# Performance work log

Measured on AMD Instinct MI355X. Metric: run time of the kernel, lower is better.

The kernel has to match this reference:

```python
import jax, jax.numpy as jnp
import numpy as np

# TripletSTDP hyperparameters (match torch defaults / init_kwargs)
TAU_PLUS = 20.0
TAU_MINUS = 20.0
TAU_X = 101.0
TAU_Y = 114.0
A_PLUS = 0.005
A_MINUS = 0.00525
A_TRIP_PLUS = 0.0001
A_TRIP_MINUS = 0.0001
DT = 1.0

B, T, N_PRE, N_POST = 32, 512, 1024, 1024


def setup_inputs() -> dict:
    key = jax.random.key(0)
    k1, k2, k3 = jax.random.split(key, 3)
    pre_spikes = jax.random.uniform(k1, (B, T, N_PRE), dtype=jnp.float32)
    post_spikes = jax.random.uniform(k2, (B, T, N_POST), dtype=jnp.float32)
    weights = jax.random.uniform(k3, (N_PRE, N_POST), dtype=jnp.float32)
    return {"pre_spikes": pre_spikes, "post_spikes": post_spikes, "weights": weights}


def reference(pre_spikes, post_spikes, weights):
    batch, time_steps, n_pre = pre_spikes.shape
    n_post = post_spikes.shape[-1]
    d_plus = jnp.exp(jnp.asarray(-DT / TAU_PLUS, dtype=pre_spikes.dtype))
    d_x = jnp.exp(jnp.asarray(-DT / TAU_X, dtype=pre_spikes.dtype))
    d_minus = jnp.exp(jnp.asarray(-DT / TAU_MINUS, dtype=pre_spikes.dtype))
    d_y = jnp.exp(jnp.asarray(-DT / TAU_Y, dtype=pre_spikes.dtype))
    inv_b = 1.0 / batch

    def step(carry, xs):
        r1, r2, o1, o2, wu = carry
        pre_t, post_t = xs  # [B, n_pre], [B, n_post]
        r1 = r1 * d_plus
        r2 = r2 * d_x
        o1 = o1 * d_minus
        o2 = o2 * d_y
        # LTP: (a_plus*r1 + a_tp*r1*r2) outer post_t, mean over batch
        wu = wu + jnp.einsum('bp,bq->pq', A_PLUS * r1 + A_TRIP_PLUS * (r1 * r2), post_t) * inv_b
        # LTD: pre_t outer (a_minus*o1 + a_tm*o1*o2), mean over batch, negated
        wu = wu - jnp.einsum('bp,bq->pq', pre_t, A_MINUS * o1 + A_TRIP_MINUS * (o1 * o2)) * inv_b
        return (r1 + pre_t, r2 + pre_t, o1 + post_t, o2 + post_t, wu), None

    init = (
        jnp.zeros((batch, n_pre), dtype=pre_spikes.dtype),
        jnp.zeros((batch, n_pre), dtype=pre_spikes.dtype),
        jnp.zeros((batch, n_post), dtype=post_spikes.dtype),
        jnp.zeros((batch, n_post), dtype=post_spikes.dtype),
        jnp.zeros_like(weights),
    )
    xs = (jnp.swapaxes(pre_spikes, 0, 1), jnp.swapaxes(post_spikes, 0, 1))  # [T,B,*]
    (r1, r2, o1, o2, wu), _ = jax.lax.scan(step, init, xs)
    return wu / time_steps
```

## Files before the change

kernel.cpp:

```cpp
#include <hip/hip_runtime.h>
#include <cstdint>
#include <cmath>

#define BDIM 256

constexpr int Bsz = 32;
constexpr int Tt  = 512;
constexpr int Nn  = 1024;
constexpr int SEG = 16;
constexpr int SLEN = 32;
constexpr int SPLITS = 8;
constexpr int NKT = (2 * Bsz * Tt / 32) / SPLITS;
constexpr float A_PLUS  = 0.005f;
constexpr float A_MINUS = 0.00525f;
constexpr float A_TP    = 0.0001f;
constexpr float A_TM    = 0.0001f;

typedef __attribute__((ext_vector_type(8))) short short8;
typedef __attribute__((ext_vector_type(4))) float float4v;

__device__ __forceinline__ unsigned short f2bf(float f) {
  unsigned u = __float_as_uint(f);
  u += 0x7fffu + ((u >> 16) & 1u);
  return (unsigned short)(u >> 16);
}

__global__ __launch_bounds__(BDIM) void trace_kernel(
    const float* __restrict__ pre, const float* __restrict__ post,
    unsigned short* __restrict__ Abuf, unsigned short* __restrict__ Bbuf,
    float d_plus, float d_x, float d_minus, float d_y)
{
  int nb   = blockIdx.x & 63;
  int b    = (blockIdx.x >> 6) & 31;
  int side = blockIdx.x >> 11;
  int tid  = threadIdx.x;
  int seg  = tid >> 4;
  int nl   = tid & 15;
  int n    = nb * 16 + nl;

  const float* sp = (side ? post : pre) + (size_t)b * Tt * Nn + n;
  float da = side ? d_minus : d_plus;
  float db = side ? d_y     : d_x;
  float c1 = side ? -A_MINUS : A_PLUS;
  float c2 = side ? -A_TM    : A_TP;
  unsigned short* dbuf = side ? Bbuf : Abuf;
  int sw = (nl >> 1) & 3;
  int t0 = seg * SLEN;

  __shared__ __align__(16) unsigned short op[SEG][2][16][32];
  float* lds1 = (float*)&op[0][0][0][0];
  float* lds2 = lds1 + SEG * 16;

  float s[SLEN];
#pragma unroll
  for (int j = 0; j < SLEN; ++j) s[j] = sp[(size_t)(t0 + j) * Nn];

  float l1 = 0.f, l2 = 0.f;
#pragma unroll
  for (int j = 0; j < SLEN; ++j) {
    l1 = l1 * da + s[j];
    l2 = l2 * db + s[j];
  }

  float dL1 = da, dL2 = db;
#pragma unroll
  for (int q = 0; q < 5; ++q) { dL1 *= dL1; dL2 *= dL2; }

  lds1[seg * 16 + nl] = l1; lds2[seg * 16 + nl] = l2;
  __syncthreads();
  float tr1 = 0.f, tr2 = 0.f;
#pragma unroll
  for (int m = 0; m < SEG - 1; ++m) {
    if (m < seg) {
      tr1 = tr1 * dL1 + lds1[m * 16 + nl];
      tr2 = tr2 * dL2 + lds2[m * 16 + nl];
    }
  }
  __syncthreads();

#pragma unroll
  for (int g2 = 0; g2 < SLEN / 16; ++g2) {
    short8 w0[2], w1[2];
#pragma unroll
    for (int j = 0; j < 16; ++j) {
      float sv = s[g2 * 16 + j];
      tr1 *= da; tr2 *= db;
      float tv = c1 * tr1 + c2 * (tr1 * tr2);
      unsigned short bs = f2bf(sv);
      unsigned short bt = f2bf(tv);
      unsigned short h0 = side ? bs : bt;
      unsigned short h1 = side ? bt : bs;
      w0[j >> 3][j & 7] = (short)h0;
      w1[j >> 3][j & 7] = (short)h1;
      tr1 += sv; tr2 += sv;
    }
    int slotbase = 2 * g2;
#pragma unroll
    for (int i = 0; i < 2; ++i) {
      int slot = slotbase + i;
      *(short8*)&op[seg][0][nl][(slot ^ sw) * 8] = w0[i];
      *(short8*)&op[seg][1][nl][(slot ^ sw) * 8] = w1[i];
    }
  }
  __syncthreads();

  int wid = tid >> 6, lane = tid & 63;
  const unsigned short* opb = &op[0][0][0][0];
  size_t bb = (size_t)b * 16;
#pragma unroll
  for (int st = 0; st < 8; ++st) {
    int r  = wid * 8 + st;
    int sg = r >> 1;
    int dX = r & 1;
    size_t ge = ((size_t)(dX * 512) + bb + sg) * 32768
              + (size_t)(nb >> 3) * 4096 + (size_t)(nb & 7) * 512 + lane * 8;
    *(short8*)(dbuf + ge) = *(const short8*)(opb + (size_t)r * 512 + lane * 8);
  }
}

#define GLL(gp, lp)                                                         \
  __builtin_amdgcn_global_load_lds(                                         \
      (const __attribute__((address_space(1))) unsigned int*)(gp),          \
      (__attribute__((address_space(3))) unsigned int*)(lp), 16, 0, 0)

#define WAITCNT_VM8 0xF78
#define WAITCNT_VM4 0xF74
#define WAITCNT_VM0 0xF70

__global__ __launch_bounds__(BDIM) void gemm_kernel(
    const unsigned short* __restrict__ Abuf, const unsigned short* __restrict__ Bbuf,
    float* __restrict__ partials)
{
  __shared__ unsigned short smem[3 * 8192];
  int tid  = threadIdx.x;
  int s    = blockIdx.x & 7;
  int tile = blockIdx.x >> 3;
  int pt   = tile & 7;
  int qt   = tile >> 3;

  float4v acc[4][4];
#pragma unroll
  for (int i = 0; i < 4; ++i)
#pragma unroll
    for (int j = 0; j < 4; ++j) acc[i][j] = (float4v){0.f, 0.f, 0.f, 0.f};

  int wid = tid >> 6, lane = tid & 63;
  int wr = wid >> 1, wc = wid & 1;
  int rA = wr * 64 + (lane & 15);
  int rB = wc * 64 + (lane & 15);
  int kg = (((lane >> 4) ^ ((lane >> 1) & 3)) * 8);

  const unsigned short* ga = Abuf + ((size_t)(s * NKT) * 8 + pt) * 4096 + tid * 8;
  const unsigned short* gb = Bbuf + ((size_t)(s * NKT) * 8 + qt) * 4096 + tid * 8;

#define ISSUE(kt_) do {                                                     \
    unsigned short* sb_ = smem + ((kt_) % 3) * 8192;                        \
    const unsigned short* a_ = ga + (size_t)(kt_) * 8 * 4096;               \
    const unsigned short* b_ = gb + (size_t)(kt_) * 8 * 4096;               \
    GLL(a_,        sb_ + tid * 8);                                          \
    GLL(a_ + 2048, sb_ + 2048 + tid * 8);                                   \
    GLL(b_,        sb_ + 4096 + tid * 8);                                   \
    GLL(b_ + 2048, sb_ + 6144 + tid * 8);                                   \
  } while (0)

  ISSUE(0);
  ISSUE(1);

  for (int kt = 0; kt < NKT; ++kt) {
    if (kt + 2 < NKT) {
      ISSUE(kt + 2);
      __builtin_amdgcn_s_waitcnt(WAITCNT_VM8);
    } else if (kt + 2 == NKT) {
      __builtin_amdgcn_s_waitcnt(WAITCNT_VM4);
    } else {
      __builtin_amdgcn_s_waitcnt(WAITCNT_VM0);
    }
    __builtin_amdgcn_s_barrier();

    const unsigned short* sb = smem + (kt % 3) * 8192;
    short8 af[4], bfv[4];
#pragma unroll
    for (int mi = 0; mi < 4; ++mi)
      af[mi] = *(const short8*)(sb + (rA + mi * 16) * 32 + kg);
#pragma unroll
    for (int ni = 0; ni < 4; ++ni)
      bfv[ni] = *(const short8*)(sb + 4096 + (rB + ni * 16) * 32 + kg);
#pragma unroll
    for (int mi = 0; mi < 4; ++mi)
#pragma unroll
      for (int ni = 0; ni < 4; ++ni)
        acc[mi][ni] = __builtin_amdgcn_mfma_f32_16x16x32_bf16(af[mi], bfv[ni], acc[mi][ni], 0, 0, 0);
  }

  float* po = partials + (size_t)s * Nn * Nn;
#pragma unroll
  for (int mi = 0; mi < 4; ++mi)
#pragma unroll
    for (int r = 0; r < 4; ++r) {
      int row = pt * 128 + wr * 64 + mi * 16 + (lane >> 4) * 4 + r;
#pragma unroll
      for (int ni = 0; ni < 4; ++ni) {
        int col = qt * 128 + wc * 64 + ni * 16 + (lane & 15);
        po[(size_t)row * Nn + col] = acc[mi][ni][r];
      }
    }
#undef ISSUE
}

__global__ __launch_bounds__(BDIM) void reduce_kernel(
    const float4v* __restrict__ partials, float4v* __restrict__ out, int S, float scale)
{
  size_t i = (size_t)blockIdx.x * BDIM + threadIdx.x;
  float4v v = (float4v){0.f, 0.f, 0.f, 0.f};
  for (int s = 0; s < S; ++s) v += partials[(size_t)s * (Nn * Nn / 4) + i];
  out[i] = v * scale;
}

extern "C" void kernel_launch(void* const* d_in, const int* in_sizes, int n_in,
                              void* d_out, int out_size, void* d_ws, size_t ws_size,
                              hipStream_t stream)
{
  const float* pre  = (const float*)d_in[0];
  const float* post = (const float*)d_in[1];
  float4v* out = (float4v*)d_out;
  char* ws = (char*)d_ws;

  size_t sizeAB = (size_t)2 * Bsz * Tt * Nn * 2;

  float* partials = (float*)ws;
  unsigned short* Abuf = (unsigned short*)(ws + (size_t)SPLITS * Nn * Nn * 4);
  unsigned short* Bbuf = (unsigned short*)(ws + (size_t)SPLITS * Nn * Nn * 4 + sizeAB);

  float d_plus  = expf(-1.0f / 20.0f);
  float d_x     = expf(-1.0f / 101.0f);
  float d_minus = expf(-1.0f / 20.0f);
  float d_y     = expf(-1.0f / 114.0f);

  trace_kernel<<<2 * Bsz * Nn / 16, BDIM, 0, stream>>>(
      pre, post, Abuf, Bbuf, d_plus, d_x, d_minus, d_y);
  gemm_kernel<<<64 * SPLITS, BDIM, 0, stream>>>(Abuf, Bbuf, partials);
  reduce_kernel<<<(Nn * Nn / 4) / BDIM, BDIM, 0, stream>>>(
      (const float4v*)partials, out, SPLITS, 1.0f / (float)(Bsz * Tt));
}
```

Baseline: 256.2 us.

## Widen trace blocks to 32 neurons with longer time segments, two-pass LDS staging

The trace kernel now gives each block 32 neurons and 8 time segments of 64 steps, instead of 16 neurons and 16 segments of 32. Global reads become wider (128 B per row per segment) and the serial cross-segment prefix shrinks. Each thread produces its 64 steps in two halves that reuse the same LDS staging buffer, with barriers between the halves, before writing the bf16 operand tiles in the layout the GEMM expects. The price is 64 floats of register state per thread, hence launch_bounds(256,4), plus an extra barrier round and half as many blocks.

```diff
diff --git a/kernel.cpp b/kernel.cpp
--- a/kernel.cpp
+++ b/kernel.cpp
@@ -7,8 +7,8 @@
 constexpr int Bsz = 32;
 constexpr int Tt  = 512;
 constexpr int Nn  = 1024;
-constexpr int SEG = 16;
-constexpr int SLEN = 32;
+constexpr int SEG = 8;
+constexpr int SLEN = 64;
 constexpr int SPLITS = 8;
 constexpr int NKT = (2 * Bsz * Tt / 32) / SPLITS;
 constexpr float A_PLUS  = 0.005f;
@@ -25,18 +25,18 @@
   return (unsigned short)(u >> 16);
 }
 
-__global__ __launch_bounds__(BDIM) void trace_kernel(
+__global__ __launch_bounds__(BDIM, 4) void trace_kernel(
     const float* __restrict__ pre, const float* __restrict__ post,
     unsigned short* __restrict__ Abuf, unsigned short* __restrict__ Bbuf,
     float d_plus, float d_x, float d_minus, float d_y)
 {
-  int nb   = blockIdx.x & 63;
-  int b    = (blockIdx.x >> 6) & 31;
-  int side = blockIdx.x >> 11;
+  int nb   = blockIdx.x & 31;
+  int b    = (blockIdx.x >> 5) & 31;
+  int side = blockIdx.x >> 10;
   int tid  = threadIdx.x;
-  int seg  = tid >> 4;
-  int nl   = tid & 15;
-  int n    = nb * 16 + nl;
+  int seg  = tid >> 5;
+  int nl   = tid & 31;
+  int n    = nb * 32 + nl;
 
   const float* sp = (side ? post : pre) + (size_t)b * Tt * Nn + n;
   float da = side ? d_minus : d_plus;
@@ -47,9 +47,9 @@
   int sw = (nl >> 1) & 3;
   int t0 = seg * SLEN;
 
-  __shared__ __align__(16) unsigned short op[SEG][2][16][32];
+  __shared__ __align__(16) unsigned short op[SEG][2][32][32];
   float* lds1 = (float*)&op[0][0][0][0];
-  float* lds2 = lds1 + SEG * 16;
+  float* lds2 = lds1 + SEG * 32;
 
   float s[SLEN];
 #pragma unroll
@@ -64,57 +64,64 @@
 
   float dL1 = da, dL2 = db;
 #pragma unroll
-  for (int q = 0; q < 5; ++q) { dL1 *= dL1; dL2 *= dL2; }
-
-  lds1[seg * 16 + nl] = l1; lds2[seg * 16 + nl] = l2;
+  for (int q = 0; q < 6; ++q) { dL1 *= dL1; dL2 *= dL2; }
+
+  lds1[seg * 32 + nl] = l1; lds2[seg * 32 + nl] = l2;
   __syncthreads();
   float tr1 = 0.f, tr2 = 0.f;
 #pragma unroll
   for (int m = 0; m < SEG - 1; ++m) {
     if (m < seg) {
-      tr1 = tr1 * dL1 + lds1[m * 16 + nl];
-      tr2 = tr2 * dL2 + lds2[m * 16 + nl];
+      tr1 = tr1 * dL1 + lds1[m * 32 + nl];
+      tr2 = tr2 * dL2 + lds2[m * 32 + nl];
     }
   }
   __syncthreads();
 
-#pragma unroll
-  for (int g2 = 0; g2 < SLEN / 16; ++g2) {
-    short8 w0[2], w1[2];
-#pragma unroll
-    for (int j = 0; j < 16; ++j) {
-      float sv = s[g2 * 16 + j];
-      tr1 *= da; tr2 *= db;
-      float tv = c1 * tr1 + c2 * (tr1 * tr2);
-      unsigned short bs = f2bf(sv);
-      unsigned short bt = f2bf(tv);
-      unsigned short h0 = side ? bs : bt;
-      unsigned short h1 = side ? bt : bs;
-      w0[j >> 3][j & 7] = (short)h0;
-      w1[j >> 3][j & 7] = (short)h1;
-      tr1 += sv; tr2 += sv;
-    }
-    int slotbase = 2 * g2;
-#pragma unroll
-    for (int i = 0; i < 2; ++i) {
-      int slot = slotbase + i;
-      *(short8*)&op[seg][0][nl][(slot ^ sw) * 8] = w0[i];
-      *(short8*)&op[seg][1][nl][(slot ^ sw) * 8] = w1[i];
-    }
-  }
-  __syncthreads();
-
   int wid = tid >> 6, lane = tid & 63;
-  const unsigned short* opb = &op[0][0][0][0];
-  size_t bb = (size_t)b * 16;
-#pragma unroll
-  for (int st = 0; st < 8; ++st) {
-    int r  = wid * 8 + st;
-    int sg = r >> 1;
-    int dX = r & 1;
-    size_t ge = ((size_t)(dX * 512) + bb + sg) * 32768
-              + (size_t)(nb >> 3) * 4096 + (size_t)(nb & 7) * 512 + lane * 8;
-    *(short8*)(dbuf + ge) = *(const short8*)(opb + (size_t)r * 512 + lane * 8);
+
+#pragma unroll
+  for (int r = 0; r < 2; ++r) {
+#pragma unroll
+    for (int g2 = 0; g2 < 2; ++g2) {
+      short8 w0[2], w1[2];
+#pragma unroll
+      for (int j = 0; j < 16; ++j) {
+        float sv = s[r * 32 + g2 * 16 + j];
+        tr1 *= da; tr2 *= db;
+        float tv = c1 * tr1 + c2 * (tr1 * tr2);
+        unsigned short bs = f2bf(sv);
+        unsigned short bt = f2bf(tv);
+        unsigned short h0 = side ? bs : bt;
+        unsigned short h1 = side ? bt : bs;
+        w0[j >> 3][j & 7] = (short)h0;
+        w1[j >> 3][j & 7] = (short)h1;
+        tr1 += sv; tr2 += sv;
+      }
+#pragma unroll
+      for (int i = 0; i < 2; ++i) {
+        int slot = g2 * 2 + i;
+        *(short8*)&op[seg][0][nl][(slot ^ sw) * 8] = w0[i];
+        *(short8*)&op[seg][1][nl][(slot ^ sw) * 8] = w1[i];
+      }
+    }
+    __syncthreads();
+
+    const unsigned short* opb = &op[0][0][0][0];
+#pragma unroll
+    for (int i = 0; i < 4; ++i) {
+      int rid = wid * 4 + i;
+      int sg  = rid >> 1;
+      int dX  = rid & 1;
+      size_t kt = (size_t)(dX * 512 + b * 16 + sg * 2 + r);
+      size_t ge = (kt * 8 + (size_t)(nb >> 2)) * 4096 + (size_t)(nb & 3) * 1024;
+#pragma unroll
+      for (int h = 0; h < 2; ++h) {
+        *(short8*)(dbuf + ge + h * 512 + lane * 8) =
+            *(const short8*)(opb + (size_t)rid * 1024 + h * 512 + lane * 8);
+      }
+    }
+    if (r == 0) __syncthreads();
   }
 }
 
@@ -236,7 +243,7 @@
   float d_minus = expf(-1.0f / 20.0f);
   float d_y     = expf(-1.0f / 114.0f);
 
-  trace_kernel<<<2 * Bsz * Nn / 16, BDIM, 0, stream>>>(
+  trace_kernel<<<2 * Bsz * Nn / 32, BDIM, 0, stream>>>(
       pre, post, Abuf, Bbuf, d_plus, d_x, d_minus, d_y);
   gemm_kernel<<<64 * SPLITS, BDIM, 0, stream>>>(Abuf, Bbuf, partials);
   reduce_kernel<<<(Nn * Nn / 4) / BDIM, BDIM, 0, stream>>>(
```

Result: faster. 243.5 us (-5.0%).
